# Performance work log

Measured on AMD Instinct MI355X. Metric: run time of the kernel, lower is better.

Reference implementation:

```python
import jax, jax.numpy as jnp
import numpy as np

# --- Mamba2Enc config (matches init_kwargs + mamba_ssm Mamba2 defaults) ---
D_IN = 1024
D_MODEL = 512
N_CLASSES = 2
NLAYERS = 2
D_STATE = 64
D_CONV = 4
EXPAND = 2
HEADDIM = 64
D_INNER = EXPAND * D_MODEL            # 1024
NHEADS = D_INNER // HEADDIM           # 16
CONV_DIM = D_INNER + 2 * D_STATE      # 1152 (ngroups=1)
D_IN_PROJ = 2 * D_INNER + 2 * D_STATE + NHEADS  # 2192
EPS = 1e-5


def setup_inputs() -> dict:
    key = jax.random.key(0)
    ks = jax.random.split(key, 10)
    def w(k, shape, sc=0.02):
        return jax.random.normal(k, shape, jnp.float32) * sc
    x = jax.random.normal(ks[0], (4, 4096, D_IN), jnp.float32)
    # fc1
    W1 = w(ks[1], (D_MODEL, D_IN))
    b1 = jnp.zeros((D_MODEL,), jnp.float32)
    # per-layer params stacked on leading NLAYERS axis
    ln_w = jnp.ones((NLAYERS, D_MODEL), jnp.float32)
    ln_b = jnp.zeros((NLAYERS, D_MODEL), jnp.float32)
    W_in = w(ks[2], (NLAYERS, D_IN_PROJ, D_MODEL))
    conv_w = w(ks[3], (NLAYERS, CONV_DIM, D_CONV), 0.1)
    conv_b = jnp.zeros((NLAYERS, CONV_DIM), jnp.float32)
    # dt_bias so that softplus(dt_bias) ~ [0.001, 0.1] (mamba init range)
    dt_bias = jax.random.uniform(ks[4], (NLAYERS, NHEADS), jnp.float32, -6.0, -2.3)
    A_log = jnp.log(jnp.tile(jnp.arange(1, NHEADS + 1, dtype=jnp.float32), (NLAYERS, 1)))
    Dskip = jnp.ones((NLAYERS, NHEADS), jnp.float32)
    norm_w = jnp.ones((NLAYERS, D_INNER), jnp.float32)
    W_out = w(ks[5], (NLAYERS, D_MODEL, D_INNER))
    # classifier
    Wc = w(ks[6], (N_CLASSES, D_MODEL))
    bc = jnp.zeros((N_CLASSES,), jnp.float32)
    return dict(x=x, W1=W1, b1=b1, ln_w=ln_w, ln_b=ln_b, W_in=W_in,
                conv_w=conv_w, conv_b=conv_b, dt_bias=dt_bias, A_log=A_log,
                Dskip=Dskip, norm_w=norm_w, W_out=W_out, Wc=Wc, bc=bc)


def _layernorm(h, w, b):
    mu = jnp.mean(h, axis=-1, keepdims=True)
    var = jnp.mean(jnp.square(h - mu), axis=-1, keepdims=True)
    return (h - mu) * jax.lax.rsqrt(var + EPS) * w + b


def _silu(x):
    return x * jax.nn.sigmoid(x)


def _mamba2(x, W_in, conv_w, conv_b, dt_bias, A_log, Dskip, norm_w, W_out):
    b, l, _ = x.shape
    zxbcdt = jnp.einsum('bld,ed->ble', x, W_in)  # (b, l, D_IN_PROJ)
    z = zxbcdt[..., :D_INNER]
    xBC = zxbcdt[..., D_INNER:D_INNER + CONV_DIM]
    dt = jax.nn.softplus(zxbcdt[..., -NHEADS:] + dt_bias)  # (b, l, h)
    # causal depthwise conv1d (kernel D_CONV) + silu
    xp = jnp.pad(xBC, ((0, 0), (D_CONV - 1, 0), (0, 0)))
    xBC = sum(xp[:, k:k + l, :] * conv_w[:, k] for k in range(D_CONV)) + conv_b
    xBC = _silu(xBC)
    xh = xBC[..., :D_INNER].reshape(b, l, NHEADS, HEADDIM)
    B = xBC[..., D_INNER:D_INNER + D_STATE]   # (b, l, n) ngroups=1
    C = xBC[..., D_INNER + D_STATE:]          # (b, l, n)
    A = -jnp.exp(A_log)                       # (h,)
    dA = jnp.exp(dt * A)                      # (b, l, h)
    dtx = dt[..., None] * xh                  # (b, l, h, p)

    def step(hstate, inp):
        dA_t, dtx_t, B_t, C_t = inp  # (b,h), (b,h,p), (b,n), (b,n)
        hstate = hstate * dA_t[:, :, None, None] + dtx_t[:, :, None, :] * B_t[:, None, :, None]
        y = jnp.einsum('bn,bhnp->bhp', C_t, hstate)
        return hstate, y

    init = jnp.zeros((b, NHEADS, D_STATE, HEADDIM), x.dtype)
    xs = (dA.transpose(1, 0, 2), dtx.transpose(1, 0, 2, 3),
          B.transpose(1, 0, 2), C.transpose(1, 0, 2))
    _, ys = jax.lax.scan(step, init, xs)      # ys: (l, b, h, p)
    y = ys.transpose(1, 0, 2, 3) + Dskip[None, None, :, None] * xh
    y = y.reshape(b, l, D_INNER)
    # RMSNormGated (norm_before_gate=False): rmsnorm(y * silu(z)) * weight
    y = y * _silu(z)
    y = y * jax.lax.rsqrt(jnp.mean(jnp.square(y), axis=-1, keepdims=True) + EPS) * norm_w
    return jnp.einsum('ble,de->bld', y, W_out)


def reference(x, W1, b1, ln_w, ln_b, W_in, conv_w, conv_b, dt_bias, A_log,
              Dskip, norm_w, W_out, Wc, bc):
    # fc1: Linear + GELU (dropout is identity at eval)
    h = jax.nn.gelu(jnp.einsum('bli,di->bld', x, W1) + b1, approximate=False)
    for i in range(NLAYERS):
        h = h + _mamba2(_layernorm(h, ln_w[i], ln_b[i]), W_in[i], conv_w[i],
                        conv_b[i], dt_bias[i], A_log[i], Dskip[i], norm_w[i], W_out[i])
    return jnp.einsum('bld,cd->blc', h, Wc) + bc
```

## Files before the change

kernel.cpp:

```cpp
#include <hip/hip_runtime.h>
#include <hip/hip_bf16.h>
#include <math.h>

#define BATCH 4
#define SEQ 4096
#define ROWS 16384
#define DIN 1024
#define DMODEL 512
#define DINNER 1024
#define DSTATE 64
#define NH 16
#define HD 64
#define CONVDIM 1152
#define DPROJ 2192
#define NPAD 2304
#define QC 64
#define NCH 64
#define LD 72

typedef __attribute__((ext_vector_type(8))) __bf16 bf16x8;
typedef __attribute__((ext_vector_type(4))) __bf16 bf16x4;
typedef __attribute__((ext_vector_type(4))) float f32x4;

__device__ __forceinline__ float siluf(float x){ return x / (1.f + __expf(-x)); }
__device__ __forceinline__ float geluf(float x){ return 0.5f*x*(1.f + erff(x*0.70710678118654752440f)); }

__device__ __forceinline__ bf16x8 scale8(bf16x8 v, float s){
  bf16x8 r;
  #pragma unroll
  for (int e = 0; e < 8; e++) r[e] = (__bf16)((float)v[e]*s);
  return r;
}

__device__ __forceinline__ void gl_lds16(const void* g, void* l){
  __builtin_amdgcn_global_load_lds((const __attribute__((address_space(1))) void*)g,
                                   (__attribute__((address_space(3))) void*)l, 16, 0, 0);
}

__global__ void cast_bf16_kernel(const float* __restrict__ src, __bf16* __restrict__ dst, long n){
  long i = (long)blockIdx.x*blockDim.x + threadIdx.x;
  long stride = (long)gridDim.x*blockDim.x;
  for (; i < n; i += stride) dst[i] = (__bf16)src[i];
}

__global__ void pad_win_kernel(const float* __restrict__ src, __bf16* __restrict__ dst){
  long total = 2L*NPAD*DMODEL;
  long i = (long)blockIdx.x*blockDim.x + threadIdx.x;
  long stride = (long)gridDim.x*blockDim.x;
  for (; i < total; i += stride){
    int k = (int)(i % DMODEL);
    int n = (int)((i / DMODEL) % NPAD);
    int l = (int)(i / ((long)DMODEL*NPAD));
    float v = (n < DPROJ) ? src[((long)l*DPROJ + n)*DMODEL + k] : 0.f;
    dst[i] = (__bf16)v;
  }
}

template<typename OutT, int EPI, int BM, int BN>
__global__ __launch_bounds__(256) void gemm_bt(const __bf16* __restrict__ A, const __bf16* __restrict__ Bm,
                                               OutT* __restrict__ C, const float* __restrict__ bias,
                                               int K, int Nc){
  constexpr int MI = BM/32, NI = BN/32;
  constexpr int CHA = BM/64;
  constexpr int CHT = (BM+BN)/64;
  __shared__ __align__(16) __bf16 As[3][BM*32];
  __shared__ __align__(16) __bf16 Bs[3][BN*32];
  int bm = blockIdx.x, bn = blockIdx.y;
  int tid = threadIdx.x;
  int lane = tid & 63, wid = tid >> 6;
  int wm = (wid >> 1)*(BM/2), wn = (wid & 1)*(BN/2);
  int lr = lane & 15, kb = lane >> 4;
  f32x4 acc[MI][NI] = {};
  const char* Ab = (const char*)A + (size_t)bm*BM*(size_t)(K*2);
  const char* Bb = (const char*)Bm + (size_t)bn*BN*(size_t)(K*2);
  int nkk = K >> 5;

  auto STAGE = [&](int kk, int buf){
    #pragma unroll
    for (int it = 0; it < CHT; it++){
      int cbase = it*4096 + wid*1024;
      int off = cbase + lane*16;
      int row = off >> 6, cb = off & 63;
      if (it < CHA) gl_lds16(Ab + (size_t)row*(K*2) + kk*64 + cb, (char*)(&As[buf][0]) + cbase);
      else          gl_lds16(Bb + (size_t)(row - BM)*(K*2) + kk*64 + cb, (char*)(&Bs[buf][0]) + (cbase - BM*64));
    }
  };

  STAGE(0, 0);
  if (nkk > 1) STAGE(1, 1);
  for (int kk = 0; kk < nkk; kk++){
    int cur = kk % 3;
    if (kk + 2 < nkk){
      STAGE(kk + 2, (kk + 2) % 3);
      asm volatile("s_waitcnt vmcnt(%0)" :: "n"(2*CHT) : "memory");
    } else if (kk + 1 < nkk){
      asm volatile("s_waitcnt vmcnt(%0)" :: "n"(CHT) : "memory");
    } else {
      asm volatile("s_waitcnt vmcnt(0)" ::: "memory");
    }
    __builtin_amdgcn_sched_barrier(0);
    __builtin_amdgcn_s_barrier();
    __builtin_amdgcn_sched_barrier(0);
    const __bf16* Asb = &As[cur][0];
    const __bf16* Bsb = &Bs[cur][0];
    bf16x8 af[MI], bfr[NI];
    #pragma unroll
    for (int mi = 0; mi < MI; mi++) af[mi] = *(const bf16x8*)(Asb + (wm + mi*16 + lr)*32 + kb*8);
    #pragma unroll
    for (int ni = 0; ni < NI; ni++) bfr[ni] = *(const bf16x8*)(Bsb + (wn + ni*16 + lr)*32 + kb*8);
    #pragma unroll
    for (int mi = 0; mi < MI; mi++)
      #pragma unroll
      for (int ni = 0; ni < NI; ni++)
        acc[mi][ni] = __builtin_amdgcn_mfma_f32_16x16x32_bf16(af[mi], bfr[ni], acc[mi][ni], 0, 0, 0);
    __builtin_amdgcn_s_barrier();
    __builtin_amdgcn_sched_barrier(0);
  }
  #pragma unroll
  for (int mi = 0; mi < MI; mi++){
    #pragma unroll
    for (int ni = 0; ni < NI; ni++){
      int r0 = bm*BM + wm + mi*16 + (lane >> 4)*4;
      int c  = bn*BN + wn + ni*16 + lr;
      if (c < Nc){
        OutT* Cp = C + (size_t)r0*Nc + c;
        #pragma unroll
        for (int j = 0; j < 4; j++){
          float v = acc[mi][ni][j];
          if (EPI == 1){ float u = v + bias[c]; v = geluf(u); }
          if (EPI == 2){ v += (float)Cp[(size_t)j*Nc]; }
          Cp[(size_t)j*Nc] = (OutT)v;
        }
      }
    }
  }
}

__global__ __launch_bounds__(256) void ln_kernel(const __bf16* __restrict__ h, const float* __restrict__ w,
                                                 const float* __restrict__ b, __bf16* __restrict__ out){
  int row = blockIdx.x*4 + (threadIdx.x >> 6);
  int lane = threadIdx.x & 63;
  const __bf16* hr = h + (size_t)row*DMODEL + lane*8;
  bf16x8 a = *(const bf16x8*)hr;
  float v[8];
  #pragma unroll
  for (int i = 0; i < 8; i++) v[i] = (float)a[i];
  float s = 0.f;
  #pragma unroll
  for (int i = 0; i < 8; i++) s += v[i];
  #pragma unroll
  for (int o = 32; o; o >>= 1) s += __shfl_xor(s, o, 64);
  float mu = s*(1.f/512.f);
  float q = 0.f;
  #pragma unroll
  for (int i = 0; i < 8; i++){ float d = v[i]-mu; q += d*d; }
  #pragma unroll
  for (int o = 32; o; o >>= 1) q += __shfl_xor(q, o, 64);
  float rs = rsqrtf(q*(1.f/512.f) + 1e-5f);
  const float* wp = w + lane*8; const float* bp = b + lane*8;
  bf16x8 o8;
  #pragma unroll
  for (int i = 0; i < 8; i++) o8[i] = (__bf16)((v[i]-mu)*rs*wp[i] + bp[i]);
  *(bf16x8*)(out + (size_t)row*DMODEL + lane*8) = o8;
}

__global__ __launch_bounds__(256) void conv_bc(const __bf16* __restrict__ zx, const float* __restrict__ cw,
                                               const float* __restrict__ cb, __bf16* __restrict__ BCc){
  int idx = blockIdx.x*256 + threadIdx.x;
  int j = idx & 127;
  long bt = idx >> 7;
  int t = (int)(bt & (SEQ-1));
  int ch = DINNER + j;
  const __bf16* src = zx + (size_t)bt*DPROJ + 2048 + j;
  float acc = cb[ch] + (float)src[0]*cw[ch*4+3];
  if (t >= 1) acc += (float)src[-1L*DPROJ]*cw[ch*4+2];
  if (t >= 2) acc += (float)src[-2L*DPROJ]*cw[ch*4+1];
  if (t >= 3) acc += (float)src[-3L*DPROJ]*cw[ch*4+0];
  BCc[idx] = (__bf16)siluf(acc);
}

__global__ __launch_bounds__(256) void dt_kernel(const __bf16* __restrict__ zx, const float* __restrict__ dt_bias,
                                                 float* __restrict__ dtT){
  int idx = blockIdx.x*256 + threadIdx.x;
  int hh = idx & (NH-1); long bt = idx >> 4;
  int b = (int)(bt >> 12); int t = (int)(bt & (SEQ-1));
  float v = (float)zx[(size_t)bt*DPROJ + (DPROJ-NH) + hh] + dt_bias[hh];
  float sp = (v > 20.f) ? v : log1pf(__expf(v));
  dtT[((size_t)b*NH + hh)*SEQ + t] = sp;
}

__global__ __launch_bounds__(128) void ssd_state(const __bf16* __restrict__ zx, const __bf16* __restrict__ BCc,
                                                 const float* __restrict__ dtT, const float* __restrict__ A_log,
                                                 const float* __restrict__ cw, const float* __restrict__ cb,
                                                 __bf16* __restrict__ Schunk, float* __restrict__ Pbuf,
                                                 __bf16* __restrict__ xhT){
  __shared__ __align__(16) __bf16 Bt_all[2][64*LD];
  __shared__ __align__(16) __bf16 Xt_all[2][64*LD];
  int widx = threadIdx.x >> 6, lane = threadIdx.x & 63;
  int c = blockIdx.x*2 + widx, h = blockIdx.y, b = blockIdx.z;
  __bf16* Bt = Bt_all[widx];
  __bf16* Xt = Xt_all[widx];
  int lr = lane & 15, kb = lane >> 4, hi4 = lane >> 4;
  long t0 = (long)c*QC;
  size_t bt0 = (size_t)b*SEQ + t0;
  int bh = b*NH + h;
  float Ac = -expf(A_log[h]);
  float dtv = dtT[(size_t)bh*SEQ + t0 + lane];
  float cum = dtv*Ac;
  #pragma unroll
  for (int off = 1; off < 64; off <<= 1){ float v = __shfl_up(cum, off, 64); if (lane >= off) cum += v; }
  float cumQ = __shfl(cum, 63, 64);
  float w = __expf(cumQ - cum) * dtv;
  {
    const __bf16* bp = BCc + bt0*128 + lane;
    for (int tb = 0; tb < 8; tb++){
      bf16x8 buf;
      #pragma unroll
      for (int u = 0; u < 8; u++){
        int t = tb*8 + u;
        float bv = (float)bp[(size_t)t*128];
        buf[u] = (__bf16)(bv * __shfl(w, t, 64));
      }
      *(bf16x8*)&Bt[lane*LD + tb*8] = buf;
    }
  }
  {
    int ch = h*HD + lane;
    float w0 = cw[ch*4], w1 = cw[ch*4+1], w2 = cw[ch*4+2], w3 = cw[ch*4+3], cbv = cb[ch];
    const __bf16* xp = zx + bt0*DPROJ + (DINNER + ch);
    float x1 = (t0 >= 1) ? (float)xp[-1L*DPROJ] : 0.f;
    float x2 = (t0 >= 2) ? (float)xp[-2L*DPROJ] : 0.f;
    float x3 = (t0 >= 3) ? (float)xp[-3L*DPROJ] : 0.f;
    __bf16* xo = xhT + ((size_t)bh*NCH + c)*4096 + lane*64;
    for (int tb = 0; tb < 8; tb++){
      bf16x8 buf;
      #pragma unroll
      for (int u = 0; u < 8; u++){
        int t = tb*8 + u;
        float x0 = (float)xp[(size_t)t*DPROJ];
        float xv = siluf(cbv + w3*x0 + w2*x1 + w1*x2 + w0*x3);
        x3 = x2; x2 = x1; x1 = x0;
        buf[u] = (__bf16)xv;
      }
      *(bf16x8*)&Xt[lane*LD + tb*8] = buf;
      *(bf16x8*)(xo + tb*8) = buf;
    }
  }
  f32x4 acc[4][4] = {};
  #pragma unroll
  for (int kk = 0; kk < 2; kk++){
    bf16x8 af[4], bfr[4];
    #pragma unroll
    for (int mi = 0; mi < 4; mi++) af[mi]  = *(bf16x8*)&Bt[(mi*16+lr)*LD + kk*32 + kb*8];
    #pragma unroll
    for (int ni = 0; ni < 4; ni++) bfr[ni] = *(bf16x8*)&Xt[(ni*16+lr)*LD + kk*32 + kb*8];
    #pragma unroll
    for (int mi = 0; mi < 4; mi++)
      #pragma unroll
      for (int ni = 0; ni < 4; ni++)
        acc[mi][ni] = __builtin_amdgcn_mfma_f32_16x16x32_bf16(af[mi], bfr[ni], acc[mi][ni], 0, 0, 0);
  }
  __bf16* Sp = Schunk + ((size_t)bh*NCH + c)*4096;
  #pragma unroll
  for (int mi = 0; mi < 4; mi++)
    #pragma unroll
    for (int ni = 0; ni < 4; ni++){
      int n0 = mi*16 + hi4*4;
      int p  = ni*16 + lr;
      bf16x4 v;
      #pragma unroll
      for (int r = 0; r < 4; r++) v[r] = (__bf16)acc[mi][ni][r];
      *(bf16x4*)&Sp[p*64 + n0] = v;
    }
  if (lane == 0) Pbuf[bh*NCH + c] = __expf(cumQ);
}

__global__ __launch_bounds__(64) void ssd_comb(__bf16* __restrict__ Schunk, const float* __restrict__ Pbuf){
  int bh = blockIdx.x >> 4;
  int eb = blockIdx.x & 15;
  int e = eb*256 + threadIdx.x*4;
  __bf16* base = Schunk + (size_t)bh*NCH*4096 + e;
  float T0 = 0.f, T1 = 0.f, T2 = 0.f, T3 = 0.f;
  for (int c = 0; c < NCH; c++){
    float P = Pbuf[bh*NCH + c];
    bf16x4* p = (bf16x4*)(base + (size_t)c*4096);
    bf16x4 s = *p;
    bf16x4 o; o[0] = (__bf16)T0; o[1] = (__bf16)T1; o[2] = (__bf16)T2; o[3] = (__bf16)T3;
    *p = o;
    T0 = T0*P + (float)s[0]; T1 = T1*P + (float)s[1];
    T2 = T2*P + (float)s[2]; T3 = T3*P + (float)s[3];
  }
}

__global__ __launch_bounds__(256) void ssd_y(const __bf16* __restrict__ BCc, const float* __restrict__ dtT,
                                             const float* __restrict__ A_log, const float* __restrict__ Dskip,
                                             const __bf16* __restrict__ xhT, const __bf16* __restrict__ Spre,
                                             __bf16* __restrict__ yout){
  __shared__ __align__(16) __bf16 Gs_all[4][64*LD];
  __shared__ float cum_all[4][64], dt_all[4][64];
  int widx = threadIdx.x >> 6, lane = threadIdx.x & 63;
  int c = blockIdx.x*4 + widx, h = blockIdx.y, b = blockIdx.z;
  __bf16* Gs = Gs_all[widx];
  float* cum_s = cum_all[widx];
  float* dt_s = dt_all[widx];
  int lr = lane & 15, kb = lane >> 4, hi4 = lane >> 4;
  long t0 = (long)c*QC;
  size_t bt0 = (size_t)b*SEQ + t0;
  int bh = b*NH + h;
  float Ac = -expf(A_log[h]);
  float Dk = Dskip[h];
  float dtv = dtT[(size_t)bh*SEQ + t0 + lane];
  float cum = dtv*Ac;
  #pragma unroll
  for (int off = 1; off < 64; off <<= 1){ float v = __shfl_up(cum, off, 64); if (lane >= off) cum += v; }
  cum_s[lane] = cum; dt_s[lane] = dtv;
  bf16x8 cf[4][2];
  #pragma unroll
  for (int ni = 0; ni < 4; ni++)
    #pragma unroll
    for (int kk = 0; kk < 2; kk++)
      cf[ni][kk] = *(const bf16x8*)&BCc[(bt0 + ni*16 + lr)*128 + 64 + kk*32 + kb*8];
  f32x4 g[4][4] = {};
  #pragma unroll
  for (int kk = 0; kk < 2; kk++){
    bf16x8 bfj[4];
    #pragma unroll
    for (int mi = 0; mi < 4; mi++) bfj[mi] = *(const bf16x8*)&BCc[(bt0 + mi*16 + lr)*128 + kk*32 + kb*8];
    #pragma unroll
    for (int mi = 0; mi < 4; mi++)
      #pragma unroll
      for (int ni = 0; ni < 4; ni++)
        g[mi][ni] = __builtin_amdgcn_mfma_f32_16x16x32_bf16(bfj[mi], cf[ni][kk], g[mi][ni], 0, 0, 0);
  }
  float cumi[4];
  #pragma unroll
  for (int ni = 0; ni < 4; ni++) cumi[ni] = cum_s[ni*16 + lr];
  #pragma unroll
  for (int mi = 0; mi < 4; mi++){
    #pragma unroll
    for (int r = 0; r < 4; r++){
      int j = mi*16 + hi4*4 + r;
      float cj = cum_s[j], dj = dt_s[j];
      #pragma unroll
      for (int ni = 0; ni < 4; ni++){
        int i = ni*16 + lr;
        float v = g[mi][ni][r];
        if (i > j)       v = v * __expf(cumi[ni] - cj) * dj;
        else if (i == j) v = v*dj + Dk;
        else             v = 0.f;
        g[mi][ni][r] = v;
      }
    }
  }
  #pragma unroll
  for (int mi = 0; mi < 4; mi++)
    #pragma unroll
    for (int ni = 0; ni < 4; ni++){
      int j0 = mi*16 + hi4*4;
      int i  = ni*16 + lr;
      bf16x4 v;
      #pragma unroll
      for (int r = 0; r < 4; r++) v[r] = (__bf16)g[mi][ni][r];
      *(bf16x4*)&Gs[i*LD + j0] = v;
    }
  const __bf16* Xp = xhT + ((size_t)bh*NCH + c)*4096;
  f32x4 y4[4][4] = {};
  #pragma unroll
  for (int kk = 0; kk < 2; kk++){
    bf16x8 af2[4], bf2[4];
    #pragma unroll
    for (int mi = 0; mi < 4; mi++) af2[mi] = *(const bf16x8*)&Xp[(mi*16+lr)*64 + kk*32 + kb*8];
    #pragma unroll
    for (int ni = 0; ni < 4; ni++) bf2[ni] = *(bf16x8*)&Gs[(ni*16+lr)*LD + kk*32 + kb*8];
    #pragma unroll
    for (int mi = 0; mi < 4; mi++)
      #pragma unroll
      for (int ni = 0; ni < 4; ni++)
        y4[mi][ni] = __builtin_amdgcn_mfma_f32_16x16x32_bf16(af2[mi], bf2[ni], y4[mi][ni], 0, 0, 0);
  }
  {
    const __bf16* Sp = Spre + ((size_t)bh*NCH + c)*4096;
    float ei[4];
    #pragma unroll
    for (int ni = 0; ni < 4; ni++) ei[ni] = __expf(cumi[ni]);
    #pragma unroll
    for (int kk = 0; kk < 2; kk++){
      bf16x8 as1[4];
      #pragma unroll
      for (int mi = 0; mi < 4; mi++) as1[mi] = *(const bf16x8*)&Sp[(mi*16+lr)*64 + kk*32 + kb*8];
      #pragma unroll
      for (int ni = 0; ni < 4; ni++){
        bf16x8 cs = scale8(cf[ni][kk], ei[ni]);
        #pragma unroll
        for (int mi = 0; mi < 4; mi++)
          y4[mi][ni] = __builtin_amdgcn_mfma_f32_16x16x32_bf16(as1[mi], cs, y4[mi][ni], 0, 0, 0);
      }
    }
  }
  #pragma unroll
  for (int mi = 0; mi < 4; mi++)
    #pragma unroll
    for (int ni = 0; ni < 4; ni++){
      int p0 = mi*16 + hi4*4;
      int i  = ni*16 + lr;
      bf16x4 v;
      #pragma unroll
      for (int r = 0; r < 4; r++) v[r] = (__bf16)y4[mi][ni][r];
      *(bf16x4*)&yout[(bt0 + i)*DINNER + h*HD + p0] = v;
    }
}

__global__ __launch_bounds__(256) void gate_rms(__bf16* __restrict__ y, const __bf16* __restrict__ zx,
                                                const float* __restrict__ nw){
  int row = blockIdx.x*4 + (threadIdx.x >> 6);
  int lane = threadIdx.x & 63;
  __bf16* yr = y + (size_t)row*DINNER + lane*16;
  const __bf16* zr = zx + (size_t)row*DPROJ + lane*16;
  bf16x8 y0 = *(const bf16x8*)yr, y1 = *(const bf16x8*)(yr+8);
  bf16x8 z0 = *(const bf16x8*)zr, z1 = *(const bf16x8*)(zr+8);
  float v[16]; float ss = 0.f;
  #pragma unroll
  for (int i = 0; i < 8; i++){ float z = (float)z0[i]; float tv = (float)y0[i]*siluf(z); v[i] = tv; ss += tv*tv; }
  #pragma unroll
  for (int i = 0; i < 8; i++){ float z = (float)z1[i]; float tv = (float)y1[i]*siluf(z); v[8+i] = tv; ss += tv*tv; }
  #pragma unroll
  for (int o = 32; o; o >>= 1) ss += __shfl_xor(ss, o, 64);
  float rs = rsqrtf(ss*(1.f/1024.f) + 1e-5f);
  const float* np = nw + lane*16;
  bf16x8 o0, o1;
  #pragma unroll
  for (int i = 0; i < 8; i++){ o0[i] = (__bf16)(v[i]*rs*np[i]); o1[i] = (__bf16)(v[8+i]*rs*np[8+i]); }
  *(bf16x8*)yr = o0; *(bf16x8*)(yr+8) = o1;
}

__global__ __launch_bounds__(256) void cls_kernel(const __bf16* __restrict__ h, const float* __restrict__ Wc,
                                                  const float* __restrict__ bc, float* __restrict__ out){
  int row = blockIdx.x*4 + (threadIdx.x >> 6);
  int lane = threadIdx.x & 63;
  const __bf16* hr = h + (size_t)row*DMODEL + lane*8;
  bf16x8 a = *(const bf16x8*)hr;
  float hv[8];
  #pragma unroll
  for (int i = 0; i < 8; i++) hv[i] = (float)a[i];
  const float* w0 = Wc + lane*8;
  const float* w1 = Wc + DMODEL + lane*8;
  float s0 = 0.f, s1 = 0.f;
  #pragma unroll
  for (int i = 0; i < 8; i++){ s0 += hv[i]*w0[i]; s1 += hv[i]*w1[i]; }
  #pragma unroll
  for (int o = 32; o; o >>= 1){ s0 += __shfl_xor(s0, o, 64); s1 += __shfl_xor(s1, o, 64); }
  if (lane == 0){ out[(size_t)row*2] = s0 + bc[0]; out[(size_t)row*2 + 1] = s1 + bc[1]; }
}

extern "C" void kernel_launch(void* const* d_in, const int* in_sizes, int n_in,
                              void* d_out, int out_size, void* d_ws, size_t ws_size,
                              hipStream_t stream){
  const float* x       = (const float*)d_in[0];
  const float* W1      = (const float*)d_in[1];
  const float* b1      = (const float*)d_in[2];
  const float* ln_w    = (const float*)d_in[3];
  const float* ln_b    = (const float*)d_in[4];
  const float* W_in    = (const float*)d_in[5];
  const float* conv_w  = (const float*)d_in[6];
  const float* conv_b  = (const float*)d_in[7];
  const float* dt_bias = (const float*)d_in[8];
  const float* A_log   = (const float*)d_in[9];
  const float* Dskip   = (const float*)d_in[10];
  const float* norm_w  = (const float*)d_in[11];
  const float* W_out   = (const float*)d_in[12];
  const float* Wc      = (const float*)d_in[13];
  const float* bc      = (const float*)d_in[14];
  float* out = (float*)d_out;
  char* ws = (char*)d_ws;

  size_t off = 0;
  auto alloc = [&](size_t bytes){ void* p = ws + off; off += (bytes + 255) & ~(size_t)255; return p; };
  char*   regionA = (char*) alloc((size_t)ROWS*DIN*2);
  __bf16* W1b     = (__bf16*)alloc((size_t)DMODEL*DIN*2);
  __bf16* Winb    = (__bf16*)alloc(2L*NPAD*DMODEL*2);
  __bf16* Woutb   = (__bf16*)alloc(2L*DMODEL*DINNER*2);
  __bf16* h       = (__bf16*)alloc((size_t)ROWS*DMODEL*2);
  __bf16* zx      = (__bf16*)alloc((size_t)ROWS*DPROJ*2);
  __bf16* BCc     = (__bf16*)alloc((size_t)ROWS*128*2);
  float*  dtT     = (float*) alloc((size_t)ROWS*NH*4);
  __bf16* ybuf    = (__bf16*)alloc((size_t)ROWS*DINNER*2);
  __bf16* xhT     = (__bf16*)alloc((size_t)ROWS*DINNER*2);
  float*  Pbuf    = (float*) alloc(64L*NCH*4);
  if (off > ws_size) return;

  __bf16* x_bf   = (__bf16*)regionA;
  __bf16* hnb    = (__bf16*)regionA;
  __bf16* Schunk = (__bf16*)regionA;

  cast_bf16_kernel<<<4096, 256, 0, stream>>>(x, x_bf, (long)ROWS*DIN);
  cast_bf16_kernel<<<512, 256, 0, stream>>>(W1, W1b, (long)DMODEL*DIN);
  cast_bf16_kernel<<<1024, 256, 0, stream>>>(W_out, Woutb, 2L*DMODEL*DINNER);
  pad_win_kernel<<<2048, 256, 0, stream>>>(W_in, Winb);

  {
    dim3 g(ROWS/64, DMODEL/128);
    gemm_bt<__bf16,1,64,128><<<g, 256, 0, stream>>>(x_bf, W1b, h, b1, DIN, DMODEL);
  }

  for (int l = 0; l < 2; l++){
    ln_kernel<<<ROWS/4, 256, 0, stream>>>(h, ln_w + l*DMODEL, ln_b + l*DMODEL, hnb);
    {
      dim3 g(ROWS/128, NPAD/128);
      gemm_bt<__bf16,0,128,128><<<g, 256, 0, stream>>>(hnb, Winb + (size_t)l*NPAD*DMODEL, zx, nullptr, DMODEL, DPROJ);
    }
    conv_bc<<<(ROWS*128)/256, 256, 0, stream>>>(zx, conv_w + l*CONVDIM*4, conv_b + l*CONVDIM, BCc);
    dt_kernel<<<(ROWS*NH)/256, 256, 0, stream>>>(zx, dt_bias + l*NH, dtT);
    {
      dim3 gs(NCH/2, NH, BATCH);
      ssd_state<<<gs, 128, 0, stream>>>(zx, BCc, dtT, A_log + l*NH,
                                        conv_w + l*CONVDIM*4, conv_b + l*CONVDIM, Schunk, Pbuf, xhT);
      ssd_comb<<<64*16, 64, 0, stream>>>(Schunk, Pbuf);
      dim3 gy(NCH/4, NH, BATCH);
      ssd_y<<<gy, 256, 0, stream>>>(BCc, dtT, A_log + l*NH, Dskip + l*NH, xhT, Schunk, ybuf);
    }
    gate_rms<<<ROWS/4, 256, 0, stream>>>(ybuf, zx, norm_w + l*DINNER);
    {
      dim3 g(ROWS/64, DMODEL/128);
      gemm_bt<__bf16,2,64,128><<<g, 256, 0, stream>>>(ybuf, Woutb + (size_t)l*DMODEL*DINNER, h, nullptr, DINNER, DMODEL);
    }
  }

  cls_kernel<<<ROWS/4, 256, 0, stream>>>(h, Wc, bc, out);
}
```

Before: 488.2 us.

## Use 512-thread triple-buffered swizzled GEMM for in_proj

Adds a new GEMM kernel with 128x256 tiles, 8 waves, a three-stage LDS ring filled by direct global-to-LDS loads with XOR swizzle, and two phases per K-step that overlap loading with MFMA. It uses explicit vmcnt waits and raised scheduling priority, and replaces the in_proj GEMM launch. The aim is to hide memory latency and raise MFMA utilisation for the largest GEMM. In exchange it uses more LDS per block (about 144KB), which lowers occupancy, and the hand-tuned waitcnt logic carries correctness risk.

Result: slower. 498.7 us (+2.2%).

```diff
diff --git a/kernel.cpp b/kernel.cpp
--- a/kernel.cpp
+++ b/kernel.cpp
@@ -122,6 +122,107 @@
     for (int ni = 0; ni < NI; ni++){
       int r0 = bm*BM + wm + mi*16 + (lane >> 4)*4;
       int c  = bn*BN + wn + ni*16 + lr;
+      if (c < Nc){
+        OutT* Cp = C + (size_t)r0*Nc + c;
+        #pragma unroll
+        for (int j = 0; j < 4; j++){
+          float v = acc[mi][ni][j];
+          if (EPI == 1){ float u = v + bias[c]; v = geluf(u); }
+          if (EPI == 2){ v += (float)Cp[(size_t)j*Nc]; }
+          Cp[(size_t)j*Nc] = (OutT)v;
+        }
+      }
+    }
+  }
+}
+
+template<typename OutT, int EPI>
+__global__ __launch_bounds__(512) void gemm_8ph(const __bf16* __restrict__ A, const __bf16* __restrict__ Bm,
+                                                OutT* __restrict__ C, const float* __restrict__ bias,
+                                                int K, int Nc){
+  __shared__ __align__(16) __bf16 Ls[3][24576];
+  int bm = blockIdx.x, bn = blockIdx.y;
+  int tid = threadIdx.x;
+  int lane = tid & 63, wid = tid >> 6;
+  int wm = (wid >> 2)*64, wn = (wid & 3)*64;
+  int lr = lane & 15, kb = lane >> 4;
+  f32x4 acc[4][4] = {};
+  const char* Ab = (const char*)A + (size_t)bm*128*(size_t)(K*2);
+  const char* Bb = (const char*)Bm + (size_t)bn*256*(size_t)(K*2);
+  int NT = K >> 6;
+
+  auto STAGEH = [&](int t, int half){
+    char* lb = (char*)&Ls[t % 3][0];
+    #pragma unroll
+    for (int it = 0; it < 3; it++){
+      int c = half*3 + it;
+      int base = c*8192 + wid*1024;
+      int off = base + lane*16;
+      if (c < 2){
+        int row = off >> 7, slot = (off >> 4) & 7;
+        gl_lds16(Ab + (size_t)row*(K*2) + (size_t)t*128 + ((slot ^ (row & 7)) << 4), lb + base);
+      } else {
+        int o2 = off - 16384;
+        int row = o2 >> 7, slot = (o2 >> 4) & 7;
+        gl_lds16(Bb + (size_t)row*(K*2) + (size_t)t*128 + ((slot ^ (row & 7)) << 4), lb + base);
+      }
+    }
+  };
+
+  STAGEH(0, 0); STAGEH(0, 1);
+  STAGEH(1, 0); STAGEH(1, 1);
+  asm volatile("s_waitcnt vmcnt(6)" ::: "memory");
+  __builtin_amdgcn_sched_barrier(0);
+  __builtin_amdgcn_s_barrier();
+  __builtin_amdgcn_sched_barrier(0);
+
+  for (int t = 0; t < NT; t++){
+    const char* bufA = (const char*)&Ls[t % 3][0];
+    const char* bufB = bufA + 16384;
+    #pragma unroll
+    for (int ph = 0; ph < 2; ph++){
+      bf16x8 af[4], bfr[4];
+      #pragma unroll
+      for (int mi = 0; mi < 4; mi++){
+        int r = wm + mi*16 + lr;
+        int s = ph*4 + kb;
+        af[mi] = *(const bf16x8*)(bufA + r*128 + ((s ^ (r & 7)) << 4));
+      }
+      #pragma unroll
+      for (int ni = 0; ni < 4; ni++){
+        int r = wn + ni*16 + lr;
+        int s = ph*4 + kb;
+        bfr[ni] = *(const bf16x8*)(bufB + r*128 + ((s ^ (r & 7)) << 4));
+      }
+      if (t + 2 < NT) STAGEH(t + 2, ph);
+      if (ph == 1){
+        if (t + 2 < NT){
+          asm volatile("s_waitcnt vmcnt(6)" ::: "memory");
+        } else if (t + 1 < NT){
+          asm volatile("s_waitcnt vmcnt(0)" ::: "memory");
+        }
+      }
+      __builtin_amdgcn_sched_barrier(0);
+      __builtin_amdgcn_s_barrier();
+      asm volatile("s_waitcnt lgkmcnt(0)" ::: "memory");
+      __builtin_amdgcn_sched_barrier(0);
+      __builtin_amdgcn_s_setprio(1);
+      #pragma unroll
+      for (int mi = 0; mi < 4; mi++)
+        #pragma unroll
+        for (int ni = 0; ni < 4; ni++)
+          acc[mi][ni] = __builtin_amdgcn_mfma_f32_16x16x32_bf16(af[mi], bfr[ni], acc[mi][ni], 0, 0, 0);
+      __builtin_amdgcn_s_setprio(0);
+      __builtin_amdgcn_s_barrier();
+      __builtin_amdgcn_sched_barrier(0);
+    }
+  }
+  #pragma unroll
+  for (int mi = 0; mi < 4; mi++){
+    #pragma unroll
+    for (int ni = 0; ni < 4; ni++){
+      int r0 = bm*128 + wm + mi*16 + (lane >> 4)*4;
+      int c  = bn*256 + wn + ni*16 + lr;
       if (c < Nc){
         OutT* Cp = C + (size_t)r0*Nc + c;
         #pragma unroll
@@ -505,8 +606,8 @@
   for (int l = 0; l < 2; l++){
     ln_kernel<<<ROWS/4, 256, 0, stream>>>(h, ln_w + l*DMODEL, ln_b + l*DMODEL, hnb);
     {
-      dim3 g(ROWS/128, NPAD/128);
-      gemm_bt<__bf16,0,128,128><<<g, 256, 0, stream>>>(hnb, Winb + (size_t)l*NPAD*DMODEL, zx, nullptr, DMODEL, DPROJ);
+      dim3 g(ROWS/128, NPAD/256);
+      gemm_8ph<__bf16,0><<<g, 512, 0, stream>>>(hnb, Winb + (size_t)l*NPAD*DMODEL, zx, nullptr, DMODEL, DPROJ);
     }
     conv_bc<<<(ROWS*128)/256, 256, 0, stream>>>(zx, conv_w + l*CONVDIM*4, conv_b + l*CONVDIM, BCc);
     dt_kernel<<<(ROWS*NH)/256, 256, 0, stream>>>(zx, dt_bias + l*NH, dtT);
```
